# Kernel optimization log

Hardware: AMD Instinct MI355X
Metric: run time of the kernel (lower is better)

The kernel has to match this reference:

```python
import jax, jax.numpy as jnp
import numpy as np

H, D, E, FOCAL, HID = 8, 32, 16, 4, 256  # heads, att_size, edge types, focal heads, hidden
SCALE = D ** -0.5
B, N = 16, 512


def setup_inputs() -> dict:
    key = jax.random.key(0)
    ks = jax.random.split(key, 16)
    f = lambda i, shape, s=1.0: jax.random.normal(ks[i], shape, jnp.float32) * s
    return {
        "q": f(0, (B, N, HID)),
        "k": f(1, (B, N, HID)),
        "v": f(2, (B, N, HID)),
        "query_edge_emb": f(3, (E, H * D), 0.1),
        "key_edge_emb": f(4, (E, H * D), 0.1),
        "edge_attr": jax.random.randint(ks[5], (B, N, N), 0, E),
        "mask": jax.random.randint(ks[6], (B, N), 0, 2).astype(bool),
        "focal_mask": jax.random.randint(ks[7], (B, N, N), 0, 2).astype(bool),
        "Wq": f(8, (H * D, HID), 0.05), "bq": jnp.zeros((H * D,), jnp.float32),
        "Wk": f(9, (H * D, HID), 0.05), "bk": jnp.zeros((H * D,), jnp.float32),
        "Wv": f(10, (H * D, HID), 0.05), "bv": jnp.zeros((H * D,), jnp.float32),
        "Wo": f(11, (HID, H * D), 0.05), "bo": jnp.zeros((HID,), jnp.float32),
    }


def reference(q, k, v, query_edge_emb, key_edge_emb, edge_attr, mask, focal_mask,
              Wq, bq, Wk, bk, Wv, bv, Wo, bo):
    b, n, _ = q.shape
    # projections -> [B, H, N, D]
    qh = (q @ Wq.T + bq).reshape(b, n, H, D).transpose(0, 2, 1, 3)
    kh = (k @ Wk.T + bk).reshape(b, n, H, D).transpose(0, 2, 1, 3)
    vh = (v @ Wv.T + bv).reshape(b, n, H, D).transpose(0, 2, 1, 3)

    # edge-type embeddings -> [H, E, D]
    qe_emb = query_edge_emb.reshape(E, H, D).transpose(1, 0, 2)
    ke_emb = key_edge_emb.reshape(E, H, D).transpose(1, 0, 2)

    # per-node score against each edge type: [B, H, N, E]
    qe = jnp.einsum('bhnd,hed->bhne', qh, qe_emb)
    ke = jnp.einsum('bhnd,hed->bhne', kh, ke_emb)

    # gather per edge type id: [B, H, N, N]
    idx = jnp.broadcast_to(edge_attr[:, None, :, :], (b, H, n, n))
    edge_bias = jnp.take_along_axis(qe, idx, axis=3) + jnp.take_along_axis(ke, idx, axis=3)

    attn = (jnp.einsum('bhid,bhjd->bhij', qh, kh) + edge_bias) * SCALE

    gh = H - FOCAL
    m_g = jnp.broadcast_to(mask[:, None, None, :], (b, gh, n, n))
    m_f = jnp.broadcast_to(focal_mask[:, None, :, :], (b, FOCAL, n, n))
    m = jnp.concatenate([m_g, m_f], axis=1)
    attn = jnp.where(m, attn, -jnp.inf)
    attn = jax.nn.softmax(attn, axis=3)

    out = jnp.einsum('bhij,bhjd->bhid', attn, vh)
    out = out.transpose(0, 2, 1, 3).reshape(b, n, H * D)
    return out @ Wo.T + bo
```

## Files before the change

kernel.cpp:

```cpp
#include <hip/hip_runtime.h>
#include <math.h>

namespace {

constexpr int B = 16, N = 512, H = 8, D = 32, E = 16, HID = 256;
constexpr float SCALE = 0.17677669529663687f;
constexpr size_t HSZ = (size_t)B * H * N * D;
constexpr size_t WSZ = (size_t)HID * HID;

typedef __attribute__((ext_vector_type(8))) short short8;
typedef __attribute__((ext_vector_type(4))) float float4v;

__device__ inline short f2bf(float x) {
  union { float f; unsigned u; } v; v.f = x;
  unsigned r = v.u + 0x7fffu + ((v.u >> 16) & 1u);
  return (short)(r >> 16);
}
__device__ inline float bf2f(unsigned short u) {
  union { unsigned u; float f; } v; v.u = ((unsigned)u) << 16; return v.f;
}

__global__ __launch_bounds__(256) void convert_kernel(
    const float* __restrict__ q, const float* __restrict__ k, const float* __restrict__ v,
    const float* __restrict__ Wq, const float* __restrict__ Wk,
    const float* __restrict__ Wv, const float* __restrict__ Wo,
    unsigned short* __restrict__ qx, unsigned short* __restrict__ kx,
    unsigned short* __restrict__ vx, unsigned short* __restrict__ wq,
    unsigned short* __restrict__ wk, unsigned short* __restrict__ wv,
    unsigned short* __restrict__ wo,
    const unsigned* __restrict__ fmask_u32, int* __restrict__ flag)
{
  if (blockIdx.x == gridDim.x - 1) {
    __shared__ unsigned wr[4];
    const int t = threadIdx.x, w = t >> 6, lane = t & 63;
    unsigned o = 0;
    for (int idx = t; idx < 4096; idx += 256) o |= fmask_u32[idx];
    o |= __shfl_xor(o, 1);  o |= __shfl_xor(o, 2);  o |= __shfl_xor(o, 4);
    o |= __shfl_xor(o, 8);  o |= __shfl_xor(o, 16); o |= __shfl_xor(o, 32);
    if (lane == 0) wr[w] = o;
    __syncthreads();
    if (t == 0) flag[0] = ((wr[0] | wr[1] | wr[2] | wr[3]) > 1u) ? 1 : 0;
    return;
  }
  constexpr size_t H4 = HSZ / 4;
  constexpr size_t W4 = WSZ / 4;
  const size_t idx = (size_t)blockIdx.x * 256 + threadIdx.x;
  const float* src; unsigned short* dst; size_t off;
  if (idx < H4)            { src = q; dst = qx; off = idx; }
  else if (idx < 2 * H4)   { src = k; dst = kx; off = idx - H4; }
  else if (idx < 3 * H4)   { src = v; dst = vx; off = idx - 2 * H4; }
  else {
    const size_t r = idx - 3 * H4;
    const int wsel = (int)(r / W4); off = r % W4;
    src = (wsel == 0) ? Wq : (wsel == 1) ? Wk : (wsel == 2) ? Wv : Wo;
    dst = (wsel == 0) ? wq : (wsel == 1) ? wk : (wsel == 2) ? wv : wo;
  }
  const float4 f = ((const float4*)src)[off];
  ushort4 o;
  o.x = (unsigned short)f2bf(f.x); o.y = (unsigned short)f2bf(f.y);
  o.z = (unsigned short)f2bf(f.z); o.w = (unsigned short)f2bf(f.w);
  ((ushort4*)dst)[off] = o;
}

__global__ __launch_bounds__(256) void gemm_qkv(
    const unsigned short* __restrict__ Xq, const unsigned short* __restrict__ Xk,
    const unsigned short* __restrict__ Xv,
    const unsigned short* __restrict__ Wq, const unsigned short* __restrict__ Wk,
    const unsigned short* __restrict__ Wv,
    const float* __restrict__ bq, const float* __restrict__ bk,
    const float* __restrict__ bv,
    unsigned short* __restrict__ qh, unsigned short* __restrict__ kh,
    unsigned short* __restrict__ vt)
{
  __shared__ __align__(16) unsigned short As[64][72];
  __shared__ __align__(16) unsigned short Bs[64][72];
  const int z = blockIdx.z;
  const unsigned short* X = (z == 0) ? Xq : (z == 1) ? Xk : Xv;
  const unsigned short* W = (z == 0) ? Wq : (z == 1) ? Wk : Wv;
  const float* bias = (z == 0) ? bq : (z == 1) ? bk : bv;

  const int m0 = blockIdx.x * 64, n0 = blockIdx.y * 64;
  const int t = threadIdx.x, lane = t & 63, w = t >> 6;
  const int quad = lane >> 4, col = lane & 15;
  const int wm = (w & 1) * 32, wn = (w >> 1) * 32;
  const int srow = t >> 2, skk = (t & 3) * 16;
  float4v acc[2][2] = {{{0,0,0,0},{0,0,0,0}},{{0,0,0,0},{0,0,0,0}}};

  for (int kit = 0; kit < 4; ++kit) {
    const int k0 = kit * 64;
    {
      const unsigned short* xp = X + (size_t)(m0 + srow) * HID + k0 + skk;
      const unsigned short* wp = W + (size_t)(n0 + srow) * HID + k0 + skk;
      *(short8*)&As[srow][skk] = *(const short8*)xp;
      *(short8*)&As[srow][skk + 8] = *(const short8*)(xp + 8);
      *(short8*)&Bs[srow][skk] = *(const short8*)wp;
      *(short8*)&Bs[srow][skk + 8] = *(const short8*)(wp + 8);
    }
    __syncthreads();
#pragma unroll
    for (int ks = 0; ks < 2; ++ks) {
      const int kk = ks * 32 + quad * 8;
      short8 a0 = *(const short8*)&As[wm + col][kk];
      short8 a1 = *(const short8*)&As[wm + 16 + col][kk];
      short8 b0 = *(const short8*)&Bs[wn + col][kk];
      short8 b1 = *(const short8*)&Bs[wn + 16 + col][kk];
      acc[0][0] = __builtin_amdgcn_mfma_f32_16x16x32_bf16(a0, b0, acc[0][0], 0, 0, 0);
      acc[0][1] = __builtin_amdgcn_mfma_f32_16x16x32_bf16(a0, b1, acc[0][1], 0, 0, 0);
      acc[1][0] = __builtin_amdgcn_mfma_f32_16x16x32_bf16(a1, b0, acc[1][0], 0, 0, 0);
      acc[1][1] = __builtin_amdgcn_mfma_f32_16x16x32_bf16(a1, b1, acc[1][1], 0, 0, 0);
    }
    __syncthreads();
  }
#pragma unroll
  for (int mt = 0; mt < 2; ++mt)
#pragma unroll
    for (int nt = 0; nt < 2; ++nt)
#pragma unroll
      for (int r = 0; r < 4; ++r) {
        const int m = m0 + wm + mt * 16 + quad * 4 + r;
        const int n = n0 + wn + nt * 16 + col;
        const float val = acc[mt][nt][r] + bias[n];
        const int b_ = m >> 9, ii = m & 511, h_ = n >> 5, d_ = n & 31;
        if (z == 2) {
          vt[((size_t)(b_ * H + h_) * D + d_) * N + ii] = (unsigned short)f2bf(val);
        } else {
          unsigned short* Yh = (z == 0) ? qh : kh;
          Yh[((size_t)(b_ * H + h_) * N + ii) * D + d_] = (unsigned short)f2bf(val);
        }
      }
}

__global__ __launch_bounds__(256) void gemm_out(
    const unsigned short* __restrict__ X, const unsigned short* __restrict__ W,
    const float* __restrict__ bias, float* __restrict__ Yf)
{
  __shared__ __align__(16) unsigned short As[64][72];
  __shared__ __align__(16) unsigned short Bs[64][72];
  const int m0 = blockIdx.x * 64, n0 = blockIdx.y * 64;
  const int t = threadIdx.x, lane = t & 63, w = t >> 6;
  const int quad = lane >> 4, col = lane & 15;
  const int wm = (w & 1) * 32, wn = (w >> 1) * 32;
  const int srow = t >> 2, skk = (t & 3) * 16;
  float4v acc[2][2] = {{{0,0,0,0},{0,0,0,0}},{{0,0,0,0},{0,0,0,0}}};

  for (int kit = 0; kit < 4; ++kit) {
    const int k0 = kit * 64;
    {
      const unsigned short* xp = X + (size_t)(m0 + srow) * HID + k0 + skk;
      const unsigned short* wp = W + (size_t)(n0 + srow) * HID + k0 + skk;
      *(short8*)&As[srow][skk] = *(const short8*)xp;
      *(short8*)&As[srow][skk + 8] = *(const short8*)(xp + 8);
      *(short8*)&Bs[srow][skk] = *(const short8*)wp;
      *(short8*)&Bs[srow][skk + 8] = *(const short8*)(wp + 8);
    }
    __syncthreads();
#pragma unroll
    for (int ks = 0; ks < 2; ++ks) {
      const int kk = ks * 32 + quad * 8;
      short8 a0 = *(const short8*)&As[wm + col][kk];
      short8 a1 = *(const short8*)&As[wm + 16 + col][kk];
      short8 b0 = *(const short8*)&Bs[wn + col][kk];
      short8 b1 = *(const short8*)&Bs[wn + 16 + col][kk];
      acc[0][0] = __builtin_amdgcn_mfma_f32_16x16x32_bf16(a0, b0, acc[0][0], 0, 0, 0);
      acc[0][1] = __builtin_amdgcn_mfma_f32_16x16x32_bf16(a0, b1, acc[0][1], 0, 0, 0);
      acc[1][0] = __builtin_amdgcn_mfma_f32_16x16x32_bf16(a1, b0, acc[1][0], 0, 0, 0);
      acc[1][1] = __builtin_amdgcn_mfma_f32_16x16x32_bf16(a1, b1, acc[1][1], 0, 0, 0);
    }
    __syncthreads();
  }
#pragma unroll
  for (int mt = 0; mt < 2; ++mt)
#pragma unroll
    for (int nt = 0; nt < 2; ++nt)
#pragma unroll
      for (int r = 0; r < 4; ++r) {
        const int m = m0 + wm + mt * 16 + quad * 4 + r;
        const int n = n0 + wn + nt * 16 + col;
        Yf[(size_t)m * HID + n] = acc[mt][nt][r] + bias[n];
      }
}

__global__ __launch_bounds__(256) void qke_kernel(
    const unsigned short* __restrict__ qh, const unsigned short* __restrict__ kh,
    const float* __restrict__ qemb, const float* __restrict__ kemb,
    float* __restrict__ qke)
{
  __shared__ float qs[512], ks[512];
  const int t = threadIdx.x;
  const int r0 = blockIdx.x * 16;
  const size_t base = (size_t)r0 * 32;
  for (int idx = t; idx < 512; idx += 256) {
    qs[idx] = bf2f(qh[base + idx]);
    ks[idx] = bf2f(kh[base + idx]);
  }
  __syncthreads();
  const int r = t >> 4, e = t & 15;
  const int h = ((r0 + r) >> 9) & 7;
  const float* qe = qemb + e * (H * D) + h * D;
  const float* ke = kemb + e * (H * D) + h * D;
  float a = 0.f;
#pragma unroll
  for (int d = 0; d < 32; ++d)
    a += qs[r * 32 + d] * qe[d] + ks[r * 32 + d] * ke[d];
  qke[(size_t)r0 * 16 + t] = a;
}

__global__ __launch_bounds__(256) void pack_kernel(
    const int* __restrict__ ea, const void* __restrict__ maskp,
    const void* __restrict__ fmaskp, const int* __restrict__ flag,
    unsigned char* __restrict__ packed)
{
  __shared__ unsigned char tl[16 * 520];
  const int it = blockIdx.x, b = blockIdx.y, t = threadIdx.x;
  const int i0 = it * 16;
  const int bf = *flag;
  const int* fm32 = (const int*)fmaskp;
  const unsigned char* fm8 = (const unsigned char*)fmaskp;
  const int* mk32 = (const int*)maskp;
  const unsigned char* mk8 = (const unsigned char*)maskp;

  for (int idx4 = t; idx4 < 2048; idx4 += 256) {
    const int m = idx4 >> 7, j4 = (idx4 & 127) * 4;
    const size_t rowoff = ((size_t)(b * N) + i0 + m) * N;
    const int4 e4 = *(const int4*)(ea + rowoff + j4);
    int fv0, fv1, fv2, fv3, mv0, mv1, mv2, mv3;
    if (bf) {
      const unsigned fw = *(const unsigned*)(fm8 + rowoff + j4);
      fv0 = fw & 0xff; fv1 = (fw >> 8) & 0xff; fv2 = (fw >> 16) & 0xff; fv3 = fw >> 24;
      const unsigned mw = *(const unsigned*)(mk8 + b * N + j4);
      mv0 = mw & 0xff; mv1 = (mw >> 8) & 0xff; mv2 = (mw >> 16) & 0xff; mv3 = mw >> 24;
    } else {
      const int4 fw = *(const int4*)(fm32 + rowoff + j4);
      fv0 = fw.x; fv1 = fw.y; fv2 = fw.z; fv3 = fw.w;
      const int4 mw = *(const int4*)(mk32 + b * N + j4);
      mv0 = mw.x; mv1 = mw.y; mv2 = mw.z; mv3 = mw.w;
    }
    const unsigned b0 = (e4.x & 15) | (fv0 ? 16u : 0u) | (mv0 ? 32u : 0u);
    const unsigned b1 = (e4.y & 15) | (fv1 ? 16u : 0u) | (mv1 ? 32u : 0u);
    const unsigned b2 = (e4.z & 15) | (fv2 ? 16u : 0u) | (mv2 ? 32u : 0u);
    const unsigned b3 = (e4.w & 15) | (fv3 ? 16u : 0u) | (mv3 ? 32u : 0u);
    *(unsigned*)&tl[m * 520 + j4] = b0 | (b1 << 8) | (b2 << 16) | (b3 << 24);
  }
  __syncthreads();
#pragma unroll
  for (int rep = 0; rep < 2; ++rep) {
    const int j = t * 2 + rep;
    unsigned wd[4];
#pragma unroll
    for (int g = 0; g < 4; ++g) {
      const unsigned c0 = tl[(g * 4 + 0) * 520 + j];
      const unsigned c1 = tl[(g * 4 + 1) * 520 + j];
      const unsigned c2 = tl[(g * 4 + 2) * 520 + j];
      const unsigned c3 = tl[(g * 4 + 3) * 520 + j];
      wd[g] = c0 | (c1 << 8) | (c2 << 16) | (c3 << 24);
    }
    *(uint4*)(packed + ((size_t)(b * 32 + it) * 512 + j) * 16) =
        make_uint4(wd[0], wd[1], wd[2], wd[3]);
  }
}

__global__ __launch_bounds__(256, 4) void attn_mfma(
    const unsigned short* __restrict__ qh, const unsigned short* __restrict__ kh,
    const unsigned short* __restrict__ vt, const float* __restrict__ qke,
    const unsigned char* __restrict__ packed, unsigned short* __restrict__ ctx)
{
  __shared__ __align__(16) unsigned short P[4][16][136];
  __shared__ float qesS[2][16][17];
  __shared__ float ored[4][2][16][33];
  __shared__ float2 wlm[4][2][16];
  __shared__ float scl[4][32];
  __shared__ float linv[32];

  const int it = blockIdx.x, p = blockIdx.y, b = blockIdx.z;
  const int i0 = it * 16;
  const int t = threadIdx.x, w = t >> 6, lane = t & 63;
  const int quad = lane >> 4, col = lane & 15;

  unsigned pk[8];
  {
    const unsigned char* pt = packed + ((size_t)(b * 32 + it) * 512) * 16;
#pragma unroll
    for (int c = 0; c < 8; ++c)
      pk[c] = *(const unsigned*)(pt + (size_t)(w * 128 + c * 16 + col) * 16 + quad * 4);
  }
#pragma unroll
  for (int rep = 0; rep < 2; ++rep) {
    const int vi = rep * 256 + t;
    const int h2 = vi >> 8, m = (vi >> 4) & 15, e = vi & 15;
    qesS[h2][m][e] =
        qke[((size_t)(b * H + p + h2 * 4) * N + i0 + m) * E + e] * SCALE;
  }
  __syncthreads();

#pragma unroll
  for (int h2 = 0; h2 < 2; ++h2) {
    const int bh = b * H + p + h2 * 4;
    const short8 qf = *(const short8*)(qh + ((size_t)bh * N + i0 + col) * D + quad * 8);

    float s[8][4];
#pragma unroll
    for (int c = 0; c < 8; ++c) {
      const int j0 = w * 128 + c * 16;
      const short8 kf = *(const short8*)(kh + ((size_t)bh * N + j0 + col) * D + quad * 8);
      float4v sc = {0, 0, 0, 0};
      sc = __builtin_amdgcn_mfma_f32_16x16x32_bf16(qf, kf, sc, 0, 0, 0);
#pragma unroll
      for (int r = 0; r < 4; ++r) {
        const int m = quad * 4 + r;
        const unsigned by = pk[c] >> (8 * r);
        const int e = by & 15;
        const int valid = h2 ? (by >> 4) & 1 : (by >> 5) & 1;
        const float sv = fmaf(sc[r], SCALE, qesS[h2][m][e]);
        s[c][r] = valid ? sv : -INFINITY;
      }
    }

    float mW[4];
#pragma unroll
    for (int r = 0; r < 4; ++r) {
      float m2 = s[0][r];
#pragma unroll
      for (int c = 1; c < 8; ++c) m2 = fmaxf(m2, s[c][r]);
      m2 = fmaxf(m2, __shfl_xor(m2, 1));
      m2 = fmaxf(m2, __shfl_xor(m2, 2));
      m2 = fmaxf(m2, __shfl_xor(m2, 4));
      m2 = fmaxf(m2, __shfl_xor(m2, 8));
      mW[r] = fmaxf(m2, -3.0e38f);
    }
#pragma unroll
    for (int r = 0; r < 4; ++r) {
      const int m = quad * 4 + r;
      float sm = 0.f;
#pragma unroll
      for (int c = 0; c < 8; ++c) {
        const float ex = __expf(s[c][r] - mW[r]);
        sm += ex;
        P[w][m][c * 16 + col] = (unsigned short)f2bf(ex);
      }
      sm += __shfl_xor(sm, 1);
      sm += __shfl_xor(sm, 2);
      sm += __shfl_xor(sm, 4);
      sm += __shfl_xor(sm, 8);
      if (col == 0) wlm[w][h2][m] = make_float2(mW[r], sm);
    }

    float4v o0 = {0, 0, 0, 0}, o1 = {0, 0, 0, 0};
#pragma unroll
    for (int c2 = 0; c2 < 4; ++c2) {
      const int kl = c2 * 32 + quad * 8;
      const short8 pf = *(const short8*)&P[w][col][kl];
      const int kg = w * 128 + kl;
      const short8 v0 = *(const short8*)(vt + ((size_t)bh * D + col) * N + kg);
      const short8 v1 = *(const short8*)(vt + ((size_t)bh * D + 16 + col) * N + kg);
      o0 = __builtin_amdgcn_mfma_f32_16x16x32_bf16(pf, v0, o0, 0, 0, 0);
      o1 = __builtin_amdgcn_mfma_f32_16x16x32_bf16(pf, v1, o1, 0, 0, 0);
    }
#pragma unroll
    for (int r = 0; r < 4; ++r) {
      ored[w][h2][quad * 4 + r][col] = o0[r];
      ored[w][h2][quad * 4 + r][col + 16] = o1[r];
    }
  }
  __syncthreads();

  if (t < 128) {
    const int u = t & 3, row = t >> 2, h2 = row >> 4, q = row & 15;
    const float2 s0 = wlm[0][h2][q], s1 = wlm[1][h2][q];
    const float2 s2 = wlm[2][h2][q], s3 = wlm[3][h2][q];
    const float mg = fmaxf(fmaxf(s0.x, s1.x), fmaxf(s2.x, s3.x));
    const float2 sw = (u == 0) ? s0 : (u == 1) ? s1 : (u == 2) ? s2 : s3;
    scl[u][row] = __expf(sw.x - mg);
    if (u == 0) {
      const float ls = s0.y * __expf(s0.x - mg) + s1.y * __expf(s1.x - mg) +
                       s2.y * __expf(s2.x - mg) + s3.y * __expf(s3.x - mg);
      linv[row] = 1.0f / ls;
    }
  }
  __syncthreads();

#pragma unroll
  for (int it2 = 0; it2 < 4; ++it2) {
    const int flat = it2 * 256 + t;
    const int h2 = flat >> 9, rem = flat & 511, q = rem >> 5, d = rem & 31;
    const int row = h2 * 16 + q;
    const float val = ored[0][h2][q][d] * scl[0][row] +
                      ored[1][h2][q][d] * scl[1][row] +
                      ored[2][h2][q][d] * scl[2][row] +
                      ored[3][h2][q][d] * scl[3][row];
    ctx[((size_t)(b * N) + i0 + q) * HID + (p + h2 * 4) * D + d] =
        (unsigned short)f2bf(val * linv[row]);
  }
}

}

extern "C" void kernel_launch(void* const* d_in, const int* in_sizes, int n_in,
                              void* d_out, int out_size, void* d_ws, size_t ws_size,
                              hipStream_t stream)
{
  const float* q    = (const float*)d_in[0];
  const float* k    = (const float*)d_in[1];
  const float* v    = (const float*)d_in[2];
  const float* qemb = (const float*)d_in[3];
  const float* kemb = (const float*)d_in[4];
  const int*   ea   = (const int*)d_in[5];
  const void*  mask = d_in[6];
  const void*  fmask= d_in[7];
  const float* Wq = (const float*)d_in[8];
  const float* bq = (const float*)d_in[9];
  const float* Wk = (const float*)d_in[10];
  const float* bk = (const float*)d_in[11];
  const float* Wv = (const float*)d_in[12];
  const float* bv = (const float*)d_in[13];
  const float* Wo = (const float*)d_in[14];
  const float* bo = (const float*)d_in[15];

  unsigned short* ws16 = (unsigned short*)d_ws;
  unsigned short* qhb = ws16;
  unsigned short* khb = qhb + HSZ;
  unsigned short* vtb = khb + HSZ;
  float* qkew = (float*)(vtb + HSZ);
  unsigned short* ctx = (unsigned short*)(qkew + (size_t)B * H * N * E);
  unsigned char* packed = (unsigned char*)(ctx + (size_t)B * N * HID);
  unsigned short* qxb = (unsigned short*)(packed + (size_t)B * N * N);
  unsigned short* kxb = qxb + HSZ;
  unsigned short* vxb = kxb + HSZ;
  unsigned short* wqb = vxb + HSZ;
  unsigned short* wkb = wqb + WSZ;
  unsigned short* wvb = wkb + WSZ;
  unsigned short* wob = wvb + WSZ;
  int* flag = (int*)(wob + WSZ);

  convert_kernel<<<6401, 256, 0, stream>>>(q, k, v, Wq, Wk, Wv, Wo,
                                           qxb, kxb, vxb, wqb, wkb, wvb, wob,
                                           (const unsigned*)fmask, flag);
  pack_kernel<<<dim3(N / 16, B), 256, 0, stream>>>(ea, mask, fmask, flag, packed);
  gemm_qkv<<<dim3((B * N) / 64, HID / 64, 3), 256, 0, stream>>>(
      qxb, kxb, vxb, wqb, wkb, wvb, bq, bk, bv, qhb, khb, vtb);
  qke_kernel<<<(B * H * N) / 16, 256, 0, stream>>>(qhb, khb, qemb, kemb, qkew);
  attn_mfma<<<dim3(N / 16, H / 2, B), 256, 0, stream>>>(qhb, khb, vtb, qkew,
                                                        packed, ctx);
  gemm_out<<<dim3((B * N) / 64, HID / 64), 256, 0, stream>>>(ctx, wob, bo, (float*)d_out);
}
```

Baseline: 212.2 us.

## Fuse mask packing into convert kernel and edge scores into attention kernel

Merges the bf16 conversion and edge/mask packing into one prep kernel, so each packing block now detects the mask format itself instead of reading a flag. It drops the separate qke kernel by computing the per-node edge-type scores inside the attention kernel from bf16 q/k rows and the edge embeddings staged in shared memory. It also transposes the V projection output through shared memory so the vt stores are coalesced. This removes two launches and a float scratch round-trip, at the cost of redundant mask-format scans and extra per-block work in attention. The edge embeddings are rounded to bf16, a small accuracy change, and the attention kernel's launch-bounds occupancy hint is dropped.

Result: faster. 181.9 us (-14.3%).

```diff
diff --git a/kernel.cpp b/kernel.cpp
--- a/kernel.cpp
+++ b/kernel.cpp
@@ -7,6 +7,7 @@
 constexpr float SCALE = 0.17677669529663687f;
 constexpr size_t HSZ = (size_t)B * H * N * D;
 constexpr size_t WSZ = (size_t)HID * HID;
+constexpr int CONV_BLOCKS = 6400;
 
 typedef __attribute__((ext_vector_type(8))) short short8;
 typedef __attribute__((ext_vector_type(4))) float float4v;
@@ -20,7 +21,7 @@
   union { unsigned u; float f; } v; v.u = ((unsigned)u) << 16; return v.f;
 }
 
-__global__ __launch_bounds__(256) void convert_kernel(
+__global__ __launch_bounds__(256) void prep_kernel(
     const float* __restrict__ q, const float* __restrict__ k, const float* __restrict__ v,
     const float* __restrict__ Wq, const float* __restrict__ Wk,
     const float* __restrict__ Wv, const float* __restrict__ Wo,
@@ -28,38 +29,92 @@
     unsigned short* __restrict__ vx, unsigned short* __restrict__ wq,
     unsigned short* __restrict__ wk, unsigned short* __restrict__ wv,
     unsigned short* __restrict__ wo,
-    const unsigned* __restrict__ fmask_u32, int* __restrict__ flag)
+    const int* __restrict__ ea, const void* __restrict__ maskp,
+    const void* __restrict__ fmaskp, unsigned char* __restrict__ packed)
 {
-  if (blockIdx.x == gridDim.x - 1) {
-    __shared__ unsigned wr[4];
-    const int t = threadIdx.x, w = t >> 6, lane = t & 63;
-    unsigned o = 0;
-    for (int idx = t; idx < 4096; idx += 256) o |= fmask_u32[idx];
-    o |= __shfl_xor(o, 1);  o |= __shfl_xor(o, 2);  o |= __shfl_xor(o, 4);
-    o |= __shfl_xor(o, 8);  o |= __shfl_xor(o, 16); o |= __shfl_xor(o, 32);
-    if (lane == 0) wr[w] = o;
-    __syncthreads();
-    if (t == 0) flag[0] = ((wr[0] | wr[1] | wr[2] | wr[3]) > 1u) ? 1 : 0;
+  __shared__ unsigned char tl[16 * 520];
+  __shared__ unsigned sdet[4];
+  const int bid = blockIdx.x, t = threadIdx.x;
+
+  if (bid < CONV_BLOCKS) {
+    constexpr size_t H4 = HSZ / 4;
+    constexpr size_t W4 = WSZ / 4;
+    const size_t idx = (size_t)bid * 256 + t;
+    const float* src; unsigned short* dst; size_t off;
+    if (idx < H4)            { src = q; dst = qx; off = idx; }
+    else if (idx < 2 * H4)   { src = k; dst = kx; off = idx - H4; }
+    else if (idx < 3 * H4)   { src = v; dst = vx; off = idx - 2 * H4; }
+    else {
+      const size_t r = idx - 3 * H4;
+      const int wsel = (int)(r / W4); off = r % W4;
+      src = (wsel == 0) ? Wq : (wsel == 1) ? Wk : (wsel == 2) ? Wv : Wo;
+      dst = (wsel == 0) ? wq : (wsel == 1) ? wk : (wsel == 2) ? wv : wo;
+    }
+    const float4 f = ((const float4*)src)[off];
+    ushort4 o;
+    o.x = (unsigned short)f2bf(f.x); o.y = (unsigned short)f2bf(f.y);
+    o.z = (unsigned short)f2bf(f.z); o.w = (unsigned short)f2bf(f.w);
+    ((ushort4*)dst)[off] = o;
     return;
   }
-  constexpr size_t H4 = HSZ / 4;
-  constexpr size_t W4 = WSZ / 4;
-  const size_t idx = (size_t)blockIdx.x * 256 + threadIdx.x;
-  const float* src; unsigned short* dst; size_t off;
-  if (idx < H4)            { src = q; dst = qx; off = idx; }
-  else if (idx < 2 * H4)   { src = k; dst = kx; off = idx - H4; }
-  else if (idx < 3 * H4)   { src = v; dst = vx; off = idx - 2 * H4; }
-  else {
-    const size_t r = idx - 3 * H4;
-    const int wsel = (int)(r / W4); off = r % W4;
-    src = (wsel == 0) ? Wq : (wsel == 1) ? Wk : (wsel == 2) ? Wv : Wo;
-    dst = (wsel == 0) ? wq : (wsel == 1) ? wk : (wsel == 2) ? wv : wo;
-  }
-  const float4 f = ((const float4*)src)[off];
-  ushort4 o;
-  o.x = (unsigned short)f2bf(f.x); o.y = (unsigned short)f2bf(f.y);
-  o.z = (unsigned short)f2bf(f.z); o.w = (unsigned short)f2bf(f.w);
-  ((ushort4*)dst)[off] = o;
+
+  const int pb = bid - CONV_BLOCKS;
+  const int it = pb & 31, b = pb >> 5;
+  const int i0 = it * 16;
+  const int w = t >> 6, lane = t & 63;
+  const unsigned* fm_u = (const unsigned*)fmaskp;
+  unsigned o = 0;
+#pragma unroll
+  for (int i = 0; i < 4; ++i) o |= fm_u[t + i * 256];
+  o |= __shfl_xor(o, 1);  o |= __shfl_xor(o, 2);  o |= __shfl_xor(o, 4);
+  o |= __shfl_xor(o, 8);  o |= __shfl_xor(o, 16); o |= __shfl_xor(o, 32);
+  if (lane == 0) sdet[w] = o;
+  __syncthreads();
+  const int bf = ((sdet[0] | sdet[1] | sdet[2] | sdet[3]) > 1u) ? 1 : 0;
+
+  const int* fm32 = (const int*)fmaskp;
+  const unsigned char* fm8 = (const unsigned char*)fmaskp;
+  const int* mk32 = (const int*)maskp;
+  const unsigned char* mk8 = (const unsigned char*)maskp;
+
+  for (int idx4 = t; idx4 < 2048; idx4 += 256) {
+    const int m = idx4 >> 7, j4 = (idx4 & 127) * 4;
+    const size_t rowoff = ((size_t)(b * N) + i0 + m) * N;
+    const int4 e4 = *(const int4*)(ea + rowoff + j4);
+    int fv0, fv1, fv2, fv3, mv0, mv1, mv2, mv3;
+    if (bf) {
+      const unsigned fw = *(const unsigned*)(fm8 + rowoff + j4);
+      fv0 = fw & 0xff; fv1 = (fw >> 8) & 0xff; fv2 = (fw >> 16) & 0xff; fv3 = fw >> 24;
+      const unsigned mw = *(const unsigned*)(mk8 + b * N + j4);
+      mv0 = mw & 0xff; mv1 = (mw >> 8) & 0xff; mv2 = (mw >> 16) & 0xff; mv3 = mw >> 24;
+    } else {
+      const int4 fw = *(const int4*)(fm32 + rowoff + j4);
+      fv0 = fw.x; fv1 = fw.y; fv2 = fw.z; fv3 = fw.w;
+      const int4 mw = *(const int4*)(mk32 + b * N + j4);
+      mv0 = mw.x; mv1 = mw.y; mv2 = mw.z; mv3 = mw.w;
+    }
+    const unsigned b0 = (e4.x & 15) | (fv0 ? 16u : 0u) | (mv0 ? 32u : 0u);
+    const unsigned b1 = (e4.y & 15) | (fv1 ? 16u : 0u) | (mv1 ? 32u : 0u);
+    const unsigned b2 = (e4.z & 15) | (fv2 ? 16u : 0u) | (mv2 ? 32u : 0u);
+    const unsigned b3 = (e4.w & 15) | (fv3 ? 16u : 0u) | (mv3 ? 32u : 0u);
+    *(unsigned*)&tl[m * 520 + j4] = b0 | (b1 << 8) | (b2 << 16) | (b3 << 24);
+  }
+  __syncthreads();
+#pragma unroll
+  for (int rep = 0; rep < 2; ++rep) {
+    const int j = t * 2 + rep;
+    unsigned wd[4];
+#pragma unroll
+    for (int g = 0; g < 4; ++g) {
+      const unsigned c0 = tl[(g * 4 + 0) * 520 + j];
+      const unsigned c1 = tl[(g * 4 + 1) * 520 + j];
+      const unsigned c2 = tl[(g * 4 + 2) * 520 + j];
+      const unsigned c3 = tl[(g * 4 + 3) * 520 + j];
+      wd[g] = c0 | (c1 << 8) | (c2 << 16) | (c3 << 24);
+    }
+    *(uint4*)(packed + ((size_t)(b * 32 + it) * 512 + j) * 16) =
+        make_uint4(wd[0], wd[1], wd[2], wd[3]);
+  }
 }
 
 __global__ __launch_bounds__(256) void gemm_qkv(
@@ -111,6 +166,28 @@
     }
     __syncthreads();
   }
+  if (z == 2) {
+#pragma unroll
+    for (int mt = 0; mt < 2; ++mt)
+#pragma unroll
+      for (int nt = 0; nt < 2; ++nt)
+#pragma unroll
+        for (int r = 0; r < 4; ++r) {
+          const int m_l = wm + mt * 16 + quad * 4 + r;
+          const int n_l = wn + nt * 16 + col;
+          As[n_l][m_l] = (unsigned short)f2bf(acc[mt][nt][r] + bias[n0 + n_l]);
+        }
+    __syncthreads();
+#pragma unroll
+    for (int rep = 0; rep < 16; ++rep) {
+      const int flat = rep * 256 + t;
+      const int n_l = flat >> 6, m_l = flat & 63;
+      const int n = n0 + n_l, m = m0 + m_l;
+      const int b_ = m >> 9, ii = m & 511, h_ = n >> 5, d_ = n & 31;
+      vt[((size_t)(b_ * H + h_) * D + d_) * N + ii] = As[n_l][m_l];
+    }
+    return;
+  }
 #pragma unroll
   for (int mt = 0; mt < 2; ++mt)
 #pragma unroll
@@ -121,12 +198,8 @@
         const int n = n0 + wn + nt * 16 + col;
         const float val = acc[mt][nt][r] + bias[n];
         const int b_ = m >> 9, ii = m & 511, h_ = n >> 5, d_ = n & 31;
-        if (z == 2) {
-          vt[((size_t)(b_ * H + h_) * D + d_) * N + ii] = (unsigned short)f2bf(val);
-        } else {
-          unsigned short* Yh = (z == 0) ? qh : kh;
-          Yh[((size_t)(b_ * H + h_) * N + ii) * D + d_] = (unsigned short)f2bf(val);
-        }
+        unsigned short* Yh = (z == 0) ? qh : kh;
+        Yh[((size_t)(b_ * H + h_) * N + ii) * D + d_] = (unsigned short)f2bf(val);
       }
 }
 
@@ -180,88 +253,10 @@
       }
 }
 
-__global__ __launch_bounds__(256) void qke_kernel(
+__global__ __launch_bounds__(256) void attn_mfma(
     const unsigned short* __restrict__ qh, const unsigned short* __restrict__ kh,
+    const unsigned short* __restrict__ vt,
     const float* __restrict__ qemb, const float* __restrict__ kemb,
-    float* __restrict__ qke)
-{
-  __shared__ float qs[512], ks[512];
-  const int t = threadIdx.x;
-  const int r0 = blockIdx.x * 16;
-  const size_t base = (size_t)r0 * 32;
-  for (int idx = t; idx < 512; idx += 256) {
-    qs[idx] = bf2f(qh[base + idx]);
-    ks[idx] = bf2f(kh[base + idx]);
-  }
-  __syncthreads();
-  const int r = t >> 4, e = t & 15;
-  const int h = ((r0 + r) >> 9) & 7;
-  const float* qe = qemb + e * (H * D) + h * D;
-  const float* ke = kemb + e * (H * D) + h * D;
-  float a = 0.f;
-#pragma unroll
-  for (int d = 0; d < 32; ++d)
-    a += qs[r * 32 + d] * qe[d] + ks[r * 32 + d] * ke[d];
-  qke[(size_t)r0 * 16 + t] = a;
-}
-
-__global__ __launch_bounds__(256) void pack_kernel(
-    const int* __restrict__ ea, const void* __restrict__ maskp,
-    const void* __restrict__ fmaskp, const int* __restrict__ flag,
-    unsigned char* __restrict__ packed)
-{
-  __shared__ unsigned char tl[16 * 520];
-  const int it = blockIdx.x, b = blockIdx.y, t = threadIdx.x;
-  const int i0 = it * 16;
-  const int bf = *flag;
-  const int* fm32 = (const int*)fmaskp;
-  const unsigned char* fm8 = (const unsigned char*)fmaskp;
-  const int* mk32 = (const int*)maskp;
-  const unsigned char* mk8 = (const unsigned char*)maskp;
-
-  for (int idx4 = t; idx4 < 2048; idx4 += 256) {
-    const int m = idx4 >> 7, j4 = (idx4 & 127) * 4;
-    const size_t rowoff = ((size_t)(b * N) + i0 + m) * N;
-    const int4 e4 = *(const int4*)(ea + rowoff + j4);
-    int fv0, fv1, fv2, fv3, mv0, mv1, mv2, mv3;
-    if (bf) {
-      const unsigned fw = *(const unsigned*)(fm8 + rowoff + j4);
-      fv0 = fw & 0xff; fv1 = (fw >> 8) & 0xff; fv2 = (fw >> 16) & 0xff; fv3 = fw >> 24;
-      const unsigned mw = *(const unsigned*)(mk8 + b * N + j4);
-      mv0 = mw & 0xff; mv1 = (mw >> 8) & 0xff; mv2 = (mw >> 16) & 0xff; mv3 = mw >> 24;
-    } else {
-      const int4 fw = *(const int4*)(fm32 + rowoff + j4);
-      fv0 = fw.x; fv1 = fw.y; fv2 = fw.z; fv3 = fw.w;
-      const int4 mw = *(const int4*)(mk32 + b * N + j4);
-      mv0 = mw.x; mv1 = mw.y; mv2 = mw.z; mv3 = mw.w;
-    }
-    const unsigned b0 = (e4.x & 15) | (fv0 ? 16u : 0u) | (mv0 ? 32u : 0u);
-    const unsigned b1 = (e4.y & 15) | (fv1 ? 16u : 0u) | (mv1 ? 32u : 0u);
-    const unsigned b2 = (e4.z & 15) | (fv2 ? 16u : 0u) | (mv2 ? 32u : 0u);
-    const unsigned b3 = (e4.w & 15) | (fv3 ? 16u : 0u) | (mv3 ? 32u : 0u);
-    *(unsigned*)&tl[m * 520 + j4] = b0 | (b1 << 8) | (b2 << 16) | (b3 << 24);
-  }
-  __syncthreads();
-#pragma unroll
-  for (int rep = 0; rep < 2; ++rep) {
-    const int j = t * 2 + rep;
-    unsigned wd[4];
-#pragma unroll
-    for (int g = 0; g < 4; ++g) {
-      const unsigned c0 = tl[(g * 4 + 0) * 520 + j];
-      const unsigned c1 = tl[(g * 4 + 1) * 520 + j];
-      const unsigned c2 = tl[(g * 4 + 2) * 520 + j];
-      const unsigned c3 = tl[(g * 4 + 3) * 520 + j];
-      wd[g] = c0 | (c1 << 8) | (c2 << 16) | (c3 << 24);
-    }
-    *(uint4*)(packed + ((size_t)(b * 32 + it) * 512 + j) * 16) =
-        make_uint4(wd[0], wd[1], wd[2], wd[3]);
-  }
-}
-
-__global__ __launch_bounds__(256, 4) void attn_mfma(
-    const unsigned short* __restrict__ qh, const unsigned short* __restrict__ kh,
-    const unsigned short* __restrict__ vt, const float* __restrict__ qke,
     const unsigned char* __restrict__ packed, unsigned short* __restrict__ ctx)
 {
   __shared__ __align__(16) unsigned short P[4][16][136];
@@ -276,6 +271,8 @@
   const int t = threadIdx.x, w = t >> 6, lane = t & 63;
   const int quad = lane >> 4, col = lane & 15;
 
+  unsigned short* SCR = &P[0][0][0];
+
   unsigned pk[8];
   {
     const unsigned char* pt = packed + ((size_t)(b * 32 + it) * 512) * 16;
@@ -283,12 +280,41 @@
     for (int c = 0; c < 8; ++c)
       pk[c] = *(const unsigned*)(pt + (size_t)(w * 128 + c * 16 + col) * 16 + quad * 4);
   }
+  {
+    const int rr = t >> 2, part = t & 3;
+    const int h2r = (rr & 31) >> 4, mr = rr & 15;
+    const unsigned short* src = (rr < 32) ? qh : kh;
+    const short8 vv = *(const short8*)(
+        src + ((size_t)(b * H + p + h2r * 4) * N + i0 + mr) * D + part * 8);
+    *(short8*)(SCR + rr * 32 + part * 8) = vv;
+    const int er = rr;
+    const int h2e = (er & 31) >> 4, ee = er & 15;
+    const float* emb = (er < 32) ? qemb : kemb;
+    const float* sp = emb + ee * 256 + (p + h2e * 4) * 32 + part * 8;
+    const float4 f1 = *(const float4*)sp, f2 = *(const float4*)(sp + 4);
+    short8 ov;
+    ov[0] = f2bf(f1.x); ov[1] = f2bf(f1.y); ov[2] = f2bf(f1.z); ov[3] = f2bf(f1.w);
+    ov[4] = f2bf(f2.x); ov[5] = f2bf(f2.y); ov[6] = f2bf(f2.z); ov[7] = f2bf(f2.w);
+    *(short8*)(SCR + 2048 + er * 32 + part * 8) = ov;
+  }
+  __syncthreads();
 #pragma unroll
   for (int rep = 0; rep < 2; ++rep) {
     const int vi = rep * 256 + t;
     const int h2 = vi >> 8, m = (vi >> 4) & 15, e = vi & 15;
-    qesS[h2][m][e] =
-        qke[((size_t)(b * H + p + h2 * 4) * N + i0 + m) * E + e] * SCALE;
+    float a = 0.f;
+#pragma unroll
+    for (int dv = 0; dv < 4; ++dv) {
+      const short8 qr = *(const short8*)(SCR + h2 * 512 + m * 32 + dv * 8);
+      const short8 kr = *(const short8*)(SCR + 1024 + h2 * 512 + m * 32 + dv * 8);
+      const short8 eq = *(const short8*)(SCR + 2048 + (h2 * 16 + e) * 32 + dv * 8);
+      const short8 ek = *(const short8*)(SCR + 3072 + (h2 * 16 + e) * 32 + dv * 8);
+#pragma unroll
+      for (int j = 0; j < 8; ++j)
+        a += bf2f((unsigned short)qr[j]) * bf2f((unsigned short)eq[j]) +
+             bf2f((unsigned short)kr[j]) * bf2f((unsigned short)ek[j]);
+    }
+    qesS[h2][m][e] = a * SCALE;
   }
   __syncthreads();
 
@@ -381,13 +407,13 @@
 #pragma unroll
   for (int it2 = 0; it2 < 4; ++it2) {
     const int flat = it2 * 256 + t;
-    const int h2 = flat >> 9, rem = flat & 511, q = rem >> 5, d = rem & 31;
-    const int row = h2 * 16 + q;
-    const float val = ored[0][h2][q][d] * scl[0][row] +
-                      ored[1][h2][q][d] * scl[1][row] +
-                      ored[2][h2][q][d] * scl[2][row] +
-                      ored[3][h2][q][d] * scl[3][row];
-    ctx[((size_t)(b * N) + i0 + q) * HID + (p + h2 * 4) * D + d] =
+    const int h2 = flat >> 9, rem = flat & 511, q2 = rem >> 5, d = rem & 31;
+    const int row = h2 * 16 + q2;
+    const float val = ored[0][h2][q2][d] * scl[0][row] +
+                      ored[1][h2][q2][d] * scl[1][row] +
+                      ored[2][h2][q2][d] * scl[2][row] +
+                      ored[3][h2][q2][d] * scl[3][row];
+    ctx[((size_t)(b * N) + i0 + q2) * HID + (p + h2 * 4) * D + d] =
         (unsigned short)f2bf(val * linv[row]);
   }
 }
@@ -419,8 +445,7 @@
   unsigned short* qhb = ws16;
   unsigned short* khb = qhb + HSZ;
   unsigned short* vtb = khb + HSZ;
-  float* qkew = (float*)(vtb + HSZ);
-  unsigned short* ctx = (unsigned short*)(qkew + (size_t)B * H * N * E);
+  unsigned short* ctx = vtb + HSZ;
   unsigned char* packed = (unsigned char*)(ctx + (size_t)B * N * HID);
   unsigned short* qxb = (unsigned short*)(packed + (size_t)B * N * N);
   unsigned short* kxb = qxb + HSZ;
@@ -429,16 +454,13 @@
   unsigned short* wkb = wqb + WSZ;
   unsigned short* wvb = wkb + WSZ;
   unsigned short* wob = wvb + WSZ;
-  int* flag = (int*)(wob + WSZ);
-
-  convert_kernel<<<6401, 256, 0, stream>>>(q, k, v, Wq, Wk, Wv, Wo,
-                                           qxb, kxb, vxb, wqb, wkb, wvb, wob,
-                                           (const unsigned*)fmask, flag);
-  pack_kernel<<<dim3(N / 16, B), 256, 0, stream>>>(ea, mask, fmask, flag, packed);
+
+  prep_kernel<<<CONV_BLOCKS + 512, 256, 0, stream>>>(
+      q, k, v, Wq, Wk, Wv, Wo, qxb, kxb, vxb, wqb, wkb, wvb, wob,
+      ea, mask, fmask, packed);
   gemm_qkv<<<dim3((B * N) / 64, HID / 64, 3), 256, 0, stream>>>(
       qxb, kxb, vxb, wqb, wkb, wvb, bq, bk, bv, qhb, khb, vtb);
-  qke_kernel<<<(B * H * N) / 16, 256, 0, stream>>>(qhb, khb, qemb, kemb, qkew);
-  attn_mfma<<<dim3(N / 16, H / 2, B), 256, 0, stream>>>(qhb, khb, vtb, qkew,
-                                                        packed, ctx);
+  attn_mfma<<<dim3(N / 16, H / 2, B), 256, 0, stream>>>(qhb, khb, vtb, qemb,
+                                                        kemb, packed, ctx);
   gemm_out<<<dim3((B * N) / 64, HID / 64), 256, 0, stream>>>(ctx, wob, bo, (float*)d_out);
 }
```
